# Performance work log

Measured on AMD Instinct MI355X. Metric: run time of the kernel, lower is better.

The kernel has to match this reference:

```python
import jax, jax.numpy as jnp
import numpy as np

N = 50000        # nodes
E = 800000       # edges (avg degree 16)
C_IN = 128
H = 256          # hidden_channels
C_OUT = 128
DEPTH = 4
K = 2            # k_hops -> K+1 = 3 TAGConv weight matrices
L = DEPTH - 1    # residual layers after layer-0 conv
EPS = 1e-5
SLOPE = 0.01     # LeakyReLU default negative slope


def setup_inputs() -> dict:
    key = jax.random.key(0)
    ks = iter(jax.random.split(key, 24))
    s = 0.02
    x = jax.random.normal(next(ks), (N, C_IN), dtype=jnp.float32)
    edge_index = jax.random.randint(next(ks), (2, E), 0, N, dtype=jnp.int64)
    edge_weight = jax.random.uniform(next(ks), (E,), dtype=jnp.float32)
    return {
        'x': x,
        'edge_index': edge_index,
        'edge_weight': edge_weight,
        'W_emb': jax.random.normal(next(ks), (C_IN, H)) * s,
        'b_emb': jnp.zeros((H,), jnp.float32),
        'conv0_W': jax.random.normal(next(ks), (K + 1, H, H)) * s,
        'conv0_b': jnp.zeros((H,), jnp.float32),
        'norm_g': jnp.ones((L, H), jnp.float32),
        'norm_b': jnp.zeros((L, H), jnp.float32),
        'conv_W': jax.random.normal(next(ks), (L, K + 1, H, H)) * s,
        'conv_b': jnp.zeros((L, H), jnp.float32),
        'mlp_W1': jax.random.normal(next(ks), (L, H, 4 * H)) * s,
        'mlp_b1': jnp.zeros((L, 4 * H), jnp.float32),
        'mlp_g': jnp.ones((L, 4 * H), jnp.float32),
        'mlp_bb': jnp.zeros((L, 4 * H), jnp.float32),
        'mlp_W2': jax.random.normal(next(ks), (L, 4 * H, H)) * s,
        'mlp_b2': jnp.zeros((L, H), jnp.float32),
        'W_out': jax.random.normal(next(ks), (H, C_OUT)) * s,
        'b_out': jnp.zeros((C_OUT,), jnp.float32),
    }


def _bn(h, g, b):
    # BatchNorm1d over node dim (training-mode batch statistics)
    m = h.mean(axis=0)
    v = h.var(axis=0)
    return g * (h - m) * jax.lax.rsqrt(v + EPS) + b


def _tagconv(h, src, dst, ew, Ws, b):
    # TAGConv (normalize=False, no self loops): sum_k (A^k h) W_k + b
    out = h @ Ws[0]
    p = h
    for k in range(1, Ws.shape[0]):
        msg = p[src] * ew[:, None]                      # [E, H] gather
        p = jax.ops.segment_sum(msg, dst, num_segments=h.shape[0])
        out = out + p @ Ws[k]
    return out + b


def reference(x, edge_index, edge_weight, W_emb, b_emb, conv0_W, conv0_b,
              norm_g, norm_b, conv_W, conv_b, mlp_W1, mlp_b1, mlp_g, mlp_bb,
              mlp_W2, mlp_b2, W_out, b_out):
    src, dst = edge_index[0], edge_index[1]
    h = x @ W_emb + b_emb                               # x_embed (t=None)
    h = _tagconv(h, src, dst, edge_weight, conv0_W, conv0_b)  # layer-0 conv only
    for l in range(norm_g.shape[0]):                    # res+ blocks
        z = jax.nn.leaky_relu(_bn(h, norm_g[l], norm_b[l]), SLOPE)
        z = _tagconv(z, src, dst, edge_weight, conv_W[l], conv_b[l])
        # pyg MLP [H, 4H, H]: Linear -> BN -> act -> Linear (plain last)
        z = jax.nn.leaky_relu(_bn(z @ mlp_W1[l] + mlp_b1[l], mlp_g[l], mlp_bb[l]), SLOPE)
        z = z @ mlp_W2[l] + mlp_b2[l]
        h = h + z                                       # residual (res=Identity)
    return h @ W_out + b_out
```

## Files before the change

### kernel.cpp

```cpp
#include <hip/hip_runtime.h>

#define HDIM 256
#define EPSV 1e-5f
#define SLOPEV 0.01f

typedef __bf16 bf16;
typedef bf16  bf16x8 __attribute__((ext_vector_type(8)));
typedef bf16  bf16x4 __attribute__((ext_vector_type(4)));
typedef float f32x4  __attribute__((ext_vector_type(4)));

#define GLD16(g, l) __builtin_amdgcn_global_load_lds( \
    (const __attribute__((address_space(1))) void*)(g), \
    (__attribute__((address_space(3))) void*)(l), 16, 0, 0)

template<bool STORE_BF16>
__global__ __launch_bounds__(256)
void gemm_bt_k(const bf16* A0, const bf16* A1, const bf16* A2, const bf16* A3,
               int nseg, int segK,
               const bf16* __restrict__ Wt,
               const float* __restrict__ bias, const bf16* __restrict__ addb,
               void* out0, void* out1, void* out2, void* out3, int ldo,
               int n_store, float* part, int n_stats)
{
    __shared__ char smem[32768];

    const int tid = threadIdx.x;
    const int wave = tid >> 6, lane = tid & 63;
    const int quad = lane >> 4, l16 = lane & 15;
    const int waveM = (wave >> 1) * 64, waveN = (wave & 1) * 64;

    int bid = blockIdx.y * gridDim.x + blockIdx.x;
    const int nwg = gridDim.x * gridDim.y;
    if ((nwg & 7) == 0) {
        const int cpx = nwg >> 3;
        bid = (bid & 7) * cpx + (bid >> 3);
    }
    const int bx = bid % gridDim.x, by = bid / gridDim.x;
    const int bm = by * 128, bn = bx * 128;
    const int K = nseg * segK;

    const bf16* segs[4] = {A0, A1, A2, A3};
    const int srow = tid >> 2;
    const int skof = (tid & 3) * 8;
    char* lAw = smem + wave * 1024;
    char* lBw = smem + 16384 + wave * 1024;

    f32x4 acc[4][4] = {};

    const int spseg = segK >> 5;
    const int T = nseg * spseg;

    auto stage = [&](int s, int kt, int b) {
        const bf16* gA = segs[s] + (size_t)(bm + srow) * segK + kt + skof;
        const bf16* gB = Wt + (size_t)(bn + srow) * K + s * segK + kt + skof;
        char* lA = lAw + b * 8192;
        char* lB = lBw + b * 8192;
        GLD16(gA,                     lA);
        GLD16(gA + (size_t)64 * segK, lA + 4096);
        GLD16(gB,                     lB);
        GLD16(gB + (size_t)64 * K,    lB + 4096);
    };

    stage(0, 0, 0);
    __syncthreads();

    int s = 0, kt = 0;
    for (int t = 0; t < T; ++t) {
        int s2 = s, kt2 = kt + 32;
        if (kt2 == segK) { s2++; kt2 = 0; }
        if (t + 1 < T) stage(s2, kt2, (t + 1) & 1);

        const bf16* pa = (const bf16*)(smem + (t & 1) * 8192)
                         + (waveM + l16) * 32 + quad * 8;
        const bf16* pb = (const bf16*)(smem + 16384 + (t & 1) * 8192)
                         + (waveN + l16) * 32 + quad * 8;
        bf16x8 a0 = *(const bf16x8*)(pa);
        bf16x8 a1 = *(const bf16x8*)(pa + 16 * 32);
        bf16x8 a2 = *(const bf16x8*)(pa + 32 * 32);
        bf16x8 a3 = *(const bf16x8*)(pa + 48 * 32);
        bf16x8 b0 = *(const bf16x8*)(pb);
        bf16x8 b1 = *(const bf16x8*)(pb + 16 * 32);
        bf16x8 b2 = *(const bf16x8*)(pb + 32 * 32);
        bf16x8 b3 = *(const bf16x8*)(pb + 48 * 32);

        acc[0][0] = __builtin_amdgcn_mfma_f32_16x16x32_bf16(a0, b0, acc[0][0], 0, 0, 0);
        acc[0][1] = __builtin_amdgcn_mfma_f32_16x16x32_bf16(a0, b1, acc[0][1], 0, 0, 0);
        acc[0][2] = __builtin_amdgcn_mfma_f32_16x16x32_bf16(a0, b2, acc[0][2], 0, 0, 0);
        acc[0][3] = __builtin_amdgcn_mfma_f32_16x16x32_bf16(a0, b3, acc[0][3], 0, 0, 0);
        acc[1][0] = __builtin_amdgcn_mfma_f32_16x16x32_bf16(a1, b0, acc[1][0], 0, 0, 0);
        acc[1][1] = __builtin_amdgcn_mfma_f32_16x16x32_bf16(a1, b1, acc[1][1], 0, 0, 0);
        acc[1][2] = __builtin_amdgcn_mfma_f32_16x16x32_bf16(a1, b2, acc[1][2], 0, 0, 0);
        acc[1][3] = __builtin_amdgcn_mfma_f32_16x16x32_bf16(a1, b3, acc[1][3], 0, 0, 0);
        acc[2][0] = __builtin_amdgcn_mfma_f32_16x16x32_bf16(a2, b0, acc[2][0], 0, 0, 0);
        acc[2][1] = __builtin_amdgcn_mfma_f32_16x16x32_bf16(a2, b1, acc[2][1], 0, 0, 0);
        acc[2][2] = __builtin_amdgcn_mfma_f32_16x16x32_bf16(a2, b2, acc[2][2], 0, 0, 0);
        acc[2][3] = __builtin_amdgcn_mfma_f32_16x16x32_bf16(a2, b3, acc[2][3], 0, 0, 0);
        acc[3][0] = __builtin_amdgcn_mfma_f32_16x16x32_bf16(a3, b0, acc[3][0], 0, 0, 0);
        acc[3][1] = __builtin_amdgcn_mfma_f32_16x16x32_bf16(a3, b1, acc[3][1], 0, 0, 0);
        acc[3][2] = __builtin_amdgcn_mfma_f32_16x16x32_bf16(a3, b2, acc[3][2], 0, 0, 0);
        acc[3][3] = __builtin_amdgcn_mfma_f32_16x16x32_bf16(a3, b3, acc[3][3], 0, 0, 0);

        __syncthreads();
        s = s2; kt = kt2;
    }

    float bv[4];
#pragma unroll
    for (int j = 0; j < 4; ++j)
        bv[j] = bias ? bias[bn + waveN + j * 16 + l16] : 0.f;
#pragma unroll
    for (int i = 0; i < 4; ++i)
#pragma unroll
        for (int j = 0; j < 4; ++j)
#pragma unroll
            for (int r = 0; r < 4; ++r)
                acc[i][j][r] += bv[j];

    void* outs[4] = {out0, out1, out2, out3};

    if (STORE_BF16) {
        char* stg = smem + wave * 4352;
        float s8[8] = {}, q8[8] = {};
        const int rsel = lane >> 3, csel = lane & 7;
#pragma unroll
        for (int ih = 0; ih < 2; ++ih) {
            __syncthreads();
#pragma unroll
            for (int iw = 0; iw < 2; ++iw) {
                int i = ih * 2 + iw;
#pragma unroll
                for (int j = 0; j < 4; ++j)
#pragma unroll
                    for (int r = 0; r < 4; ++r)
                        *(bf16*)(stg + ((iw * 16 + quad * 4 + r) * 68 + j * 16 + l16) * 2)
                            = (bf16)acc[i][j][r];
            }
            __syncthreads();
#pragma unroll
            for (int rr = 0; rr < 4; ++rr) {
                int rl = rsel + rr * 8;
                bf16x4 lo = *(const bf16x4*)(stg + (rl * 68 + csel * 8) * 2);
                bf16x4 hi = *(const bf16x4*)(stg + (rl * 68 + csel * 8 + 4) * 2);
                int rowg = bm + waveM + ih * 32 + rl;
                int colg = bn + waveN + csel * 8;
                int cseg = colg >> 8, cloc = colg & 255;
                size_t idx = (size_t)rowg * ldo + cloc;
                float f[8];
#pragma unroll
                for (int u = 0; u < 4; ++u) { f[u] = (float)lo[u]; f[4 + u] = (float)hi[u]; }
                if (addb) {
                    bf16x8 o = *(const bf16x8*)(addb + idx);
#pragma unroll
                    for (int u = 0; u < 8; ++u) f[u] += (float)o[u];
                }
                bf16x8 w;
#pragma unroll
                for (int u = 0; u < 8; ++u) w[u] = (bf16)f[u];
                if (rowg < n_store) *(bf16x8*)((bf16*)outs[cseg] + idx) = w;
                if (part && rowg < n_stats) {
#pragma unroll
                    for (int u = 0; u < 8; ++u) { s8[u] += f[u]; q8[u] += f[u] * f[u]; }
                }
            }
        }
        if (part) {
#pragma unroll
            for (int m = 8; m <= 32; m <<= 1)
#pragma unroll
                for (int u = 0; u < 8; ++u) {
                    s8[u] += __shfl_xor(s8[u], m, 64);
                    q8[u] += __shfl_xor(q8[u], m, 64);
                }
            __syncthreads();
            float* Ls = (float*)smem;
            float* Lq = Ls + 256;
            if (rsel == 0) {
#pragma unroll
                for (int u = 0; u < 8; ++u) {
                    Ls[wave * 64 + csel * 8 + u] = s8[u];
                    Lq[wave * 64 + csel * 8 + u] = q8[u];
                }
            }
            __syncthreads();
            if (tid < 128) {
                int hi = tid >> 6, c6 = tid & 63;
                float sv = Ls[hi * 64 + c6] + Ls[(hi + 2) * 64 + c6];
                float qv = Lq[hi * 64 + c6] + Lq[(hi + 2) * 64 + c6];
                int Mtot = gridDim.x * 128;
                int colg = bn + tid;
                part[(size_t)by * Mtot + colg] = sv;
                part[(size_t)(gridDim.y + by) * Mtot + colg] = qv;
            }
        }
    } else {
#pragma unroll
        for (int i = 0; i < 4; ++i)
#pragma unroll
            for (int j = 0; j < 4; ++j) {
                int colg = bn + waveN + j * 16 + l16;
                int cseg = colg >> 8, cloc = colg & 255;
#pragma unroll
                for (int r = 0; r < 4; ++r) {
                    int rowg = bm + waveM + i * 16 + quad * 4 + r;
                    if (rowg < n_store)
                        ((float*)outs[cseg])[(size_t)rowg * ldo + cloc] = acc[i][j][r];
                }
            }
    }
}

__global__ __launch_bounds__(256)
void finalize_k(const float* __restrict__ part, int GY, int M,
                const float* __restrict__ g, const float* __restrict__ bb,
                float* __restrict__ coef, float invn)
{
    const int c = blockIdx.x;
    const int t = threadIdx.x;
    float s = 0.f, q = 0.f;
    const float* ps = part + c;
    const float* pq = part + (size_t)GY * M + c;
    for (int i = t; i < GY; i += 256) {
        s += ps[(size_t)i * M];
        q += pq[(size_t)i * M];
    }
#pragma unroll
    for (int m = 1; m <= 32; m <<= 1) {
        s += __shfl_xor(s, m, 64);
        q += __shfl_xor(q, m, 64);
    }
    __shared__ float Ls[4], Lq[4];
    const int w = t >> 6, l = t & 63;
    if (l == 0) { Ls[w] = s; Lq[w] = q; }
    __syncthreads();
    if (t == 0) {
        s = Ls[0] + Ls[1] + Ls[2] + Ls[3];
        q = Lq[0] + Lq[1] + Lq[2] + Lq[3];
        float mean = s * invn;
        float var  = q * invn - mean * mean;
        float a = g[c] * rsqrtf(var + EPSV);
        coef[c]     = a;
        coef[M + c] = bb[c] - mean * a;
    }
}

__global__ __launch_bounds__(256)
void transpose_cvt_k(const float* __restrict__ src, bf16* __restrict__ dst,
                     int Kseg, int M, int G)
{
    __shared__ float t[32][33];
    const int z = blockIdx.z;
    src += (size_t)z * Kseg * M;
    const int ldd = G * Kseg;
    dst += (size_t)(z / G) * M * ldd + (size_t)(z % G) * Kseg;
    const int tM = blockIdx.x * 32, tK = blockIdx.y * 32;
    const int tx = threadIdx.x & 31, ty = threadIdx.x >> 5;
#pragma unroll
    for (int r = 0; r < 4; ++r)
        t[ty + r * 8][tx] = src[(size_t)(tK + ty + r * 8) * M + tM + tx];
    __syncthreads();
#pragma unroll
    for (int r = 0; r < 4; ++r)
        dst[(size_t)(tM + ty + r * 8) * ldd + tK + tx] = (bf16)t[tx][ty + r * 8];
}

__global__ __launch_bounds__(256)
void cvt_bf_k(const float* __restrict__ src, bf16* __restrict__ dst, long n4)
{
    long i = (long)blockIdx.x * blockDim.x + threadIdx.x;
    if (i >= n4) return;
    float4 v = ((const float4*)src)[i];
    bf16x4 o; o[0] = (bf16)v.x; o[1] = (bf16)v.y; o[2] = (bf16)v.z; o[3] = (bf16)v.w;
    ((bf16x4*)dst)[i] = o;
}

__global__ __launch_bounds__(256)
void deg_k(const int* __restrict__ dst, int* __restrict__ deg, int E)
{
    int e = blockIdx.x * blockDim.x + threadIdx.x;
    if (e < E) atomicAdd(&deg[dst[e]], 1);
}

__global__ __launch_bounds__(256)
void blocksum_k(const int* __restrict__ deg, int* __restrict__ bsum, int N)
{
    int i = blockIdx.x * 256 + threadIdx.x;
    int v = (i < N) ? deg[i] : 0;
#pragma unroll
    for (int m = 1; m <= 32; m <<= 1) v += __shfl_xor(v, m, 64);
    __shared__ int Ls[4];
    if ((threadIdx.x & 63) == 0) Ls[threadIdx.x >> 6] = v;
    __syncthreads();
    if (threadIdx.x == 0) bsum[blockIdx.x] = Ls[0] + Ls[1] + Ls[2] + Ls[3];
}

__global__ __launch_bounds__(256)
void topscan_k(const int* __restrict__ bsum, int* __restrict__ boff, int nb)
{
    __shared__ int s[256];
    int t = threadIdx.x;
    int v = (t < nb) ? bsum[t] : 0;
    s[t] = v;
    __syncthreads();
    for (int off = 1; off < 256; off <<= 1) {
        int u = (t >= off) ? s[t - off] : 0;
        __syncthreads();
        s[t] += u;
        __syncthreads();
    }
    if (t < nb) boff[t] = s[t] - v;
}

__global__ __launch_bounds__(256)
void scatterscan_k(int* __restrict__ deg_wp, const int* __restrict__ boff,
                   int* __restrict__ rowptr, int N)
{
    __shared__ int s[256];
    int t = threadIdx.x;
    int i = blockIdx.x * 256 + t;
    int v = (i < N) ? deg_wp[i] : 0;
    s[t] = v;
    __syncthreads();
    for (int off = 1; off < 256; off <<= 1) {
        int u = (t >= off) ? s[t - off] : 0;
        __syncthreads();
        s[t] += u;
        __syncthreads();
    }
    if (i < N) {
        int incl = s[t] + boff[blockIdx.x];
        rowptr[i + 1] = incl;
        deg_wp[i] = incl - v;
        if (i == 0) rowptr[0] = 0;
    }
}

__global__ __launch_bounds__(256)
void reorder_k(const int* __restrict__ src, const int* __restrict__ dst,
               const float* __restrict__ ew, int* __restrict__ wp,
               int* __restrict__ col, float* __restrict__ wgt, int E)
{
    int e = blockIdx.x * blockDim.x + threadIdx.x;
    if (e >= E) return;
    int d = dst[e];
    int pos = atomicAdd(&wp[d], 1);
    col[pos] = src[e];
    wgt[pos] = ew[e];
}

__global__ __launch_bounds__(256)
void spmm_pull_k(const bf16* __restrict__ P, const int* __restrict__ rowptr,
                 const int* __restrict__ col, const float* __restrict__ wgt,
                 bf16* __restrict__ Q, int N)
{
    int node = blockIdx.x * 8 + (threadIdx.x >> 5);
    int l = threadIdx.x & 31;
    if (node >= N) return;
    int e = rowptr[node], end = rowptr[node + 1];
    float acc[8] = {};
    for (; e + 1 < end; e += 2) {
        int   s0 = col[e], s1 = col[e + 1];
        float w0 = wgt[e], w1 = wgt[e + 1];
        bf16x8 v0 = *(const bf16x8*)(P + (size_t)s0 * HDIM + l * 8);
        bf16x8 v1 = *(const bf16x8*)(P + (size_t)s1 * HDIM + l * 8);
#pragma unroll
        for (int u = 0; u < 8; ++u)
            acc[u] += (float)v0[u] * w0 + (float)v1[u] * w1;
    }
    if (e < end) {
        int s0 = col[e]; float w0 = wgt[e];
        bf16x8 v0 = *(const bf16x8*)(P + (size_t)s0 * HDIM + l * 8);
#pragma unroll
        for (int u = 0; u < 8; ++u) acc[u] += (float)v0[u] * w0;
    }
    bf16x8 o;
#pragma unroll
    for (int u = 0; u < 8; ++u) o[u] = (bf16)acc[u];
    *(bf16x8*)(Q + (size_t)node * HDIM + l * 8) = o;
}

__global__ __launch_bounds__(256)
void apply_bn_k(const bf16* __restrict__ X, const float* __restrict__ coef,
                bf16* __restrict__ Y, int n)
{
    __shared__ float aL[256], bL[256];
    const int tid = threadIdx.x;
    aL[tid] = coef[tid]; bL[tid] = coef[256 + tid];
    __syncthreads();
    long n4 = (long)n * 64;
    for (long i = (long)blockIdx.x * 256 + tid; i < n4; i += (long)gridDim.x * 256) {
        bf16x4 v = ((const bf16x4*)X)[i];
        int c4 = (int)(i & 63) * 4;
        float r0 = fmaf((float)v[0], aL[c4 + 0], bL[c4 + 0]); r0 = r0 > 0.f ? r0 : SLOPEV * r0;
        float r1 = fmaf((float)v[1], aL[c4 + 1], bL[c4 + 1]); r1 = r1 > 0.f ? r1 : SLOPEV * r1;
        float r2 = fmaf((float)v[2], aL[c4 + 2], bL[c4 + 2]); r2 = r2 > 0.f ? r2 : SLOPEV * r2;
        float r3 = fmaf((float)v[3], aL[c4 + 3], bL[c4 + 3]); r3 = r3 > 0.f ? r3 : SLOPEV * r3;
        bf16x4 o; o[0] = (bf16)r0; o[1] = (bf16)r1; o[2] = (bf16)r2; o[3] = (bf16)r3;
        ((bf16x4*)Y)[i] = o;
    }
}

__global__ __launch_bounds__(256)
void apply_bn4_k(bf16* X0, bf16* X1, bf16* X2, bf16* X3,
                 const float* __restrict__ coef, int n)
{
    __shared__ float aL[1024], bL[1024];
    const int tid = threadIdx.x;
#pragma unroll
    for (int q = 0; q < 4; ++q) {
        int c = q * 256 + tid;
        aL[c] = coef[c]; bL[c] = coef[1024 + c];
    }
    __syncthreads();
    bf16* Xs[4] = {X0, X1, X2, X3};
    long per = (long)n * 64;
    long stride = (long)gridDim.x * 256;
    for (int q = 0; q < 4; ++q) {
        bf16* X = Xs[q];
        int cbase = q * 256;
        for (long i = (long)blockIdx.x * 256 + tid; i < per; i += stride) {
            bf16x4 v = ((const bf16x4*)X)[i];
            int c4 = cbase + (int)(i & 63) * 4;
            float r0 = fmaf((float)v[0], aL[c4 + 0], bL[c4 + 0]); r0 = r0 > 0.f ? r0 : SLOPEV * r0;
            float r1 = fmaf((float)v[1], aL[c4 + 1], bL[c4 + 1]); r1 = r1 > 0.f ? r1 : SLOPEV * r1;
            float r2 = fmaf((float)v[2], aL[c4 + 2], bL[c4 + 2]); r2 = r2 > 0.f ? r2 : SLOPEV * r2;
            float r3 = fmaf((float)v[3], aL[c4 + 3], bL[c4 + 3]); r3 = r3 > 0.f ? r3 : SLOPEV * r3;
            bf16x4 o; o[0] = (bf16)r0; o[1] = (bf16)r1; o[2] = (bf16)r2; o[3] = (bf16)r3;
            ((bf16x4*)X)[i] = o;
        }
    }
}

struct GemmArgs {
    const bf16 *A0, *A1, *A2, *A3; int nseg, segK;
    const bf16* Wt; const float* bias; const bf16* addb;
    void *o0, *o1, *o2, *o3; int ldo, M, n_store;
    float* part; int n_stats;
};

static void gemm(hipStream_t st, const GemmArgs& a, int GY, bool store_bf16)
{
    dim3 g(a.M / 128, GY), b(256);
    if (store_bf16)
        gemm_bt_k<true><<<g, b, 0, st>>>(a.A0, a.A1, a.A2, a.A3, a.nseg, a.segK,
            a.Wt, a.bias, a.addb, a.o0, a.o1, a.o2, a.o3, a.ldo, a.n_store,
            a.part, a.n_stats);
    else
        gemm_bt_k<false><<<g, b, 0, st>>>(a.A0, a.A1, a.A2, a.A3, a.nseg, a.segK,
            a.Wt, a.bias, a.addb, a.o0, a.o1, a.o2, a.o3, a.ldo, a.n_store,
            a.part, a.n_stats);
}

extern "C" void kernel_launch(void* const* d_in, const int* in_sizes, int n_in,
                              void* d_out, int out_size, void* d_ws, size_t ws_size,
                              hipStream_t stream)
{
    const float* x       = (const float*)d_in[0];
    const int*   ei      = (const int*)d_in[1];
    const float* ew      = (const float*)d_in[2];
    const float* W_emb   = (const float*)d_in[3];
    const float* b_emb   = (const float*)d_in[4];
    const float* conv0_W = (const float*)d_in[5];
    const float* conv0_b = (const float*)d_in[6];
    const float* norm_g  = (const float*)d_in[7];
    const float* norm_b  = (const float*)d_in[8];
    const float* conv_W  = (const float*)d_in[9];
    const float* conv_b  = (const float*)d_in[10];
    const float* mlp_W1  = (const float*)d_in[11];
    const float* mlp_b1  = (const float*)d_in[12];
    const float* mlp_g   = (const float*)d_in[13];
    const float* mlp_bb  = (const float*)d_in[14];
    const float* mlp_W2  = (const float*)d_in[15];
    const float* mlp_b2  = (const float*)d_in[16];
    const float* W_out   = (const float*)d_in[17];
    const float* b_out   = (const float*)d_in[18];

    const int N = in_sizes[0] / 128;
    const int E = in_sizes[2];
    const int* srcI = ei;
    const int* dstI = ei + E;
    const int N_pad = ((N + 127) / 128) * 128;
    const int GY = N_pad / 128;
    const int NB = (N + 255) / 256;

    const size_t NHp = (size_t)N_pad * HDIM;
    bf16* xb = (bf16*)d_ws;
    bf16* hb = xb + (size_t)N_pad * 128;
    bf16* cb = hb + NHp;
    bf16* p1 = cb + NHp;
    bf16* p2 = p1 + NHp;
    bf16* e1 = p2 + NHp;
    bf16* e2 = e1 + NHp;
    bf16* wa = e2 + NHp;
    bf16* Wt_emb   = wa;
    bf16* Wt_conv0 = wa + 32768;
    bf16* Wt_conv  = wa + 229376;
    bf16* Wt_mlp1  = wa + 819200;
    bf16* Wt_mlp2  = wa + 1605632;
    bf16* Wt_out   = wa + 2392064;
    float* cf_h   = (float*)(wa + 2424832);
    float* cf_m   = cf_h + 512;
    float* partb  = cf_m + 2048;
    int*   rowptr = (int*)(partb + 2 * (size_t)GY * 1024);
    int*   wp     = rowptr + (N + 1);
    int*   col    = wp + N;
    float* wgt    = (float*)(col + E);
    int*   bsum   = (int*)(wgt + E);
    int*   boff   = bsum + 256;

    const float invn = 1.0f / (float)N;
    dim3 pg((N + 7) / 8), pb(256);

    hipMemsetAsync(wp, 0, (size_t)N * 4, stream);
    deg_k<<<dim3((E + 255) / 256), dim3(256), 0, stream>>>(dstI, wp, E);
    blocksum_k<<<dim3(NB), dim3(256), 0, stream>>>(wp, bsum, N);
    topscan_k<<<dim3(1), dim3(256), 0, stream>>>(bsum, boff, NB);
    scatterscan_k<<<dim3(NB), dim3(256), 0, stream>>>(wp, boff, rowptr, N);
    reorder_k<<<dim3((E + 255) / 256), dim3(256), 0, stream>>>(srcI, dstI, ew, wp, col, wgt, E);

    cvt_bf_k<<<dim3((N * 32 + 255) / 256), dim3(256), 0, stream>>>(x, xb, (long)N * 32);
    transpose_cvt_k<<<dim3(8, 4, 1), dim3(256), 0, stream>>>(W_emb, Wt_emb, 128, 256, 1);
    transpose_cvt_k<<<dim3(8, 8, 3), dim3(256), 0, stream>>>(conv0_W, Wt_conv0, 256, 256, 3);
    transpose_cvt_k<<<dim3(8, 8, 9), dim3(256), 0, stream>>>(conv_W, Wt_conv, 256, 256, 3);
    transpose_cvt_k<<<dim3(32, 8, 3), dim3(256), 0, stream>>>(mlp_W1, Wt_mlp1, 256, 1024, 1);
    transpose_cvt_k<<<dim3(8, 32, 3), dim3(256), 0, stream>>>(mlp_W2, Wt_mlp2, 1024, 256, 1);
    transpose_cvt_k<<<dim3(4, 8, 1), dim3(256), 0, stream>>>(W_out, Wt_out, 256, 128, 1);

    {
        GemmArgs a{xb, xb, xb, xb, 1, 128, Wt_emb, b_emb, nullptr,
                   cb, cb, cb, cb, HDIM, 256, N_pad, nullptr, 0};
        gemm(stream, a, GY, true);
    }

    spmm_pull_k<<<pg, pb, 0, stream>>>(cb, rowptr, col, wgt, p1, N);
    spmm_pull_k<<<pg, pb, 0, stream>>>(p1, rowptr, col, wgt, p2, N);
    {
        GemmArgs a{cb, p1, p2, p2, 3, 256, Wt_conv0, conv0_b, nullptr,
                   hb, hb, hb, hb, HDIM, 256, N_pad, partb, N};
        gemm(stream, a, GY, true);
    }
    finalize_k<<<dim3(256), dim3(256), 0, stream>>>(partb, GY, 256, norm_g, norm_b, cf_h, invn);

    for (int l = 0; l < 3; ++l) {
        apply_bn_k<<<dim3(1024), dim3(256), 0, stream>>>(hb, cf_h, e1, N);

        spmm_pull_k<<<pg, pb, 0, stream>>>(e1, rowptr, col, wgt, p1, N);
        spmm_pull_k<<<pg, pb, 0, stream>>>(p1, rowptr, col, wgt, p2, N);
        {
            GemmArgs a{e1, p1, p2, p2, 3, 256, Wt_conv + (size_t)l * 196608,
                       conv_b + l * 256, nullptr, cb, cb, cb, cb, HDIM, 256, N_pad,
                       nullptr, 0};
            gemm(stream, a, GY, true);
        }

        {
            GemmArgs a{cb, cb, cb, cb, 1, 256, Wt_mlp1 + (size_t)l * 262144,
                       mlp_b1 + (size_t)l * 1024, nullptr, p1, p2, e1, e2, HDIM, 1024,
                       N_pad, partb, N};
            gemm(stream, a, GY, true);
        }
        finalize_k<<<dim3(1024), dim3(256), 0, stream>>>(partb, GY, 1024,
                                                         mlp_g + (size_t)l * 1024,
                                                         mlp_bb + (size_t)l * 1024, cf_m, invn);

        apply_bn4_k<<<dim3(2048), dim3(256), 0, stream>>>(p1, p2, e1, e2, cf_m, N);

        {
            GemmArgs a{p1, p2, e1, e2, 4, 256, Wt_mlp2 + (size_t)l * 262144,
                       mlp_b2 + l * 256, hb, hb, hb, hb, hb, HDIM, 256, N_pad,
                       (l < 2) ? partb : nullptr, N};
            gemm(stream, a, GY, true);
        }
        if (l < 2)
            finalize_k<<<dim3(256), dim3(256), 0, stream>>>(partb, GY, 256,
                                                            norm_g + (l + 1) * 256,
                                                            norm_b + (l + 1) * 256, cf_h, invn);
    }

    {
        GemmArgs a{hb, hb, hb, hb, 1, 256, Wt_out, b_out, nullptr,
                   d_out, d_out, d_out, d_out, 128, 128, N, nullptr, 0};
        gemm(stream, a, GY, false);
    }
}
```

Before: 1.394 ms.

## Deepen GEMM LDS pipeline to four stages with explicit vmcnt waits

Replaces the double-buffered LDS staging in the bf16 MFMA GEMM with a 4-buffer ring that keeps three tiles in flight. It uses manual s_waitcnt vmcnt counts and a single barrier per iteration in place of a trailing __syncthreads. It also raises wave priority around the MFMA block. The aim is to hide global-to-LDS load latency better. In exchange LDS per block doubles to 64KB, which may reduce occupancy, and it relies on the ring depth to avoid overwriting a buffer other waves are still reading.

```diff
diff --git a/kernel.cpp b/kernel.cpp
--- a/kernel.cpp
+++ b/kernel.cpp
@@ -22,7 +22,7 @@
                void* out0, void* out1, void* out2, void* out3, int ldo,
                int n_store, float* part, int n_stats)
 {
-    __shared__ char smem[32768];
+    __shared__ char smem[65536];
 
     const int tid = threadIdx.x;
     const int wave = tid >> 6, lane = tid & 63;
@@ -42,37 +42,43 @@
     const bf16* segs[4] = {A0, A1, A2, A3};
     const int srow = tid >> 2;
     const int skof = (tid & 3) * 8;
-    char* lAw = smem + wave * 1024;
-    char* lBw = smem + 16384 + wave * 1024;
 
     f32x4 acc[4][4] = {};
 
-    const int spseg = segK >> 5;
-    const int T = nseg * spseg;
+    const int T = (nseg * segK) >> 5;
 
     auto stage = [&](int s, int kt, int b) {
         const bf16* gA = segs[s] + (size_t)(bm + srow) * segK + kt + skof;
         const bf16* gB = Wt + (size_t)(bn + srow) * K + s * segK + kt + skof;
-        char* lA = lAw + b * 8192;
-        char* lB = lBw + b * 8192;
+        char* lA = smem + b * 8192 + wave * 1024;
+        char* lB = smem + 32768 + b * 8192 + wave * 1024;
         GLD16(gA,                     lA);
         GLD16(gA + (size_t)64 * segK, lA + 4096);
         GLD16(gB,                     lB);
         GLD16(gB + (size_t)64 * K,    lB + 4096);
     };
 
-    stage(0, 0, 0);
-    __syncthreads();
-
-    int s = 0, kt = 0;
+    int ss = 0, kk = 0;
+    for (int i = 0; i < 3; ++i) {
+        stage(ss, kk, i);
+        kk += 32; if (kk == segK) { kk = 0; ++ss; }
+    }
+
     for (int t = 0; t < T; ++t) {
-        int s2 = s, kt2 = kt + 32;
-        if (kt2 == segK) { s2++; kt2 = 0; }
-        if (t + 1 < T) stage(s2, kt2, (t + 1) & 1);
-
-        const bf16* pa = (const bf16*)(smem + (t & 1) * 8192)
+        const int rem = T - t;
+        if (rem >= 3)      asm volatile("s_waitcnt vmcnt(8)" ::: "memory");
+        else if (rem == 2) asm volatile("s_waitcnt vmcnt(4)" ::: "memory");
+        else               asm volatile("s_waitcnt vmcnt(0)" ::: "memory");
+        __builtin_amdgcn_s_barrier();
+
+        if (t + 3 < T) {
+            stage(ss, kk, (t + 3) & 3);
+            kk += 32; if (kk == segK) { kk = 0; ++ss; }
+        }
+
+        const bf16* pa = (const bf16*)(smem + (t & 3) * 8192)
                          + (waveM + l16) * 32 + quad * 8;
-        const bf16* pb = (const bf16*)(smem + 16384 + (t & 1) * 8192)
+        const bf16* pb = (const bf16*)(smem + 32768 + (t & 3) * 8192)
                          + (waveN + l16) * 32 + quad * 8;
         bf16x8 a0 = *(const bf16x8*)(pa);
         bf16x8 a1 = *(const bf16x8*)(pa + 16 * 32);
@@ -83,6 +89,7 @@
         bf16x8 b2 = *(const bf16x8*)(pb + 32 * 32);
         bf16x8 b3 = *(const bf16x8*)(pb + 48 * 32);
 
+        __builtin_amdgcn_s_setprio(1);
         acc[0][0] = __builtin_amdgcn_mfma_f32_16x16x32_bf16(a0, b0, acc[0][0], 0, 0, 0);
         acc[0][1] = __builtin_amdgcn_mfma_f32_16x16x32_bf16(a0, b1, acc[0][1], 0, 0, 0);
         acc[0][2] = __builtin_amdgcn_mfma_f32_16x16x32_bf16(a0, b2, acc[0][2], 0, 0, 0);
@@ -99,9 +106,7 @@
         acc[3][1] = __builtin_amdgcn_mfma_f32_16x16x32_bf16(a3, b1, acc[3][1], 0, 0, 0);
         acc[3][2] = __builtin_amdgcn_mfma_f32_16x16x32_bf16(a3, b2, acc[3][2], 0, 0, 0);
         acc[3][3] = __builtin_amdgcn_mfma_f32_16x16x32_bf16(a3, b3, acc[3][3], 0, 0, 0);
-
-        __syncthreads();
-        s = s2; kt = kt2;
+        __builtin_amdgcn_s_setprio(0);
     }
 
     float bv[4];
```

Result: slower. 1.544 ms (+10.7%).

## Shrink GEMM tile to 128x64, add occupancy hint, and unroll SpMM gather by 4

Applied to the files above, without the earlier changes.

The GEMM kernel's block tile drops from 128x128 to 128x64. This halves the accumulator registers and cuts shared memory to 24KB, and launch_bounds now asks for 4 blocks per CU. The goal is more occupancy and more blocks for latency hiding, at the cost of lower arithmetic intensity and more A-tile reloads. Per-wave epilogue barriers are removed and BN stats become a template parameter. Separately, the SpMM pull loop gets a 4-way unrolled gather so more independent loads are in flight.

```diff
diff --git a/kernel.cpp b/kernel.cpp
--- a/kernel.cpp
+++ b/kernel.cpp
@@ -13,8 +13,8 @@
     (const __attribute__((address_space(1))) void*)(g), \
     (__attribute__((address_space(3))) void*)(l), 16, 0, 0)
 
-template<bool STORE_BF16>
-__global__ __launch_bounds__(256)
+template<bool STORE_BF16, bool STATS>
+__global__ __launch_bounds__(256, 4)
 void gemm_bt_k(const bf16* A0, const bf16* A1, const bf16* A2, const bf16* A3,
                int nseg, int segK,
                const bf16* __restrict__ Wt,
@@ -22,12 +22,12 @@
                void* out0, void* out1, void* out2, void* out3, int ldo,
                int n_store, float* part, int n_stats)
 {
-    __shared__ char smem[32768];
+    __shared__ char smem[24576];
 
     const int tid = threadIdx.x;
     const int wave = tid >> 6, lane = tid & 63;
     const int quad = lane >> 4, l16 = lane & 15;
-    const int waveM = (wave >> 1) * 64, waveN = (wave & 1) * 64;
+    const int waveM = (wave >> 1) * 64, waveN = (wave & 1) * 32;
 
     int bid = blockIdx.y * gridDim.x + blockIdx.x;
     const int nwg = gridDim.x * gridDim.y;
@@ -36,29 +36,25 @@
         bid = (bid & 7) * cpx + (bid >> 3);
     }
     const int bx = bid % gridDim.x, by = bid / gridDim.x;
-    const int bm = by * 128, bn = bx * 128;
+    const int bm = by * 128, bn = bx * 64;
     const int K = nseg * segK;
 
     const bf16* segs[4] = {A0, A1, A2, A3};
     const int srow = tid >> 2;
     const int skof = (tid & 3) * 8;
-    char* lAw = smem + wave * 1024;
-    char* lBw = smem + 16384 + wave * 1024;
-
-    f32x4 acc[4][4] = {};
-
-    const int spseg = segK >> 5;
-    const int T = nseg * spseg;
+
+    f32x4 acc[4][2] = {};
+
+    const int T = K >> 5;
 
     auto stage = [&](int s, int kt, int b) {
         const bf16* gA = segs[s] + (size_t)(bm + srow) * segK + kt + skof;
         const bf16* gB = Wt + (size_t)(bn + srow) * K + s * segK + kt + skof;
-        char* lA = lAw + b * 8192;
-        char* lB = lBw + b * 8192;
+        char* lA = smem + b * 8192 + wave * 1024;
+        char* lB = smem + 16384 + b * 4096 + wave * 1024;
         GLD16(gA,                     lA);
         GLD16(gA + (size_t)64 * segK, lA + 4096);
         GLD16(gB,                     lB);
-        GLD16(gB + (size_t)64 * K,    lB + 4096);
     };
 
     stage(0, 0, 0);
@@ -72,7 +68,7 @@
 
         const bf16* pa = (const bf16*)(smem + (t & 1) * 8192)
                          + (waveM + l16) * 32 + quad * 8;
-        const bf16* pb = (const bf16*)(smem + 16384 + (t & 1) * 8192)
+        const bf16* pb = (const bf16*)(smem + 16384 + (t & 1) * 4096)
                          + (waveN + l16) * 32 + quad * 8;
         bf16x8 a0 = *(const bf16x8*)(pa);
         bf16x8 a1 = *(const bf16x8*)(pa + 16 * 32);
@@ -80,38 +76,28 @@
         bf16x8 a3 = *(const bf16x8*)(pa + 48 * 32);
         bf16x8 b0 = *(const bf16x8*)(pb);
         bf16x8 b1 = *(const bf16x8*)(pb + 16 * 32);
-        bf16x8 b2 = *(const bf16x8*)(pb + 32 * 32);
-        bf16x8 b3 = *(const bf16x8*)(pb + 48 * 32);
 
         acc[0][0] = __builtin_amdgcn_mfma_f32_16x16x32_bf16(a0, b0, acc[0][0], 0, 0, 0);
         acc[0][1] = __builtin_amdgcn_mfma_f32_16x16x32_bf16(a0, b1, acc[0][1], 0, 0, 0);
-        acc[0][2] = __builtin_amdgcn_mfma_f32_16x16x32_bf16(a0, b2, acc[0][2], 0, 0, 0);
-        acc[0][3] = __builtin_amdgcn_mfma_f32_16x16x32_bf16(a0, b3, acc[0][3], 0, 0, 0);
         acc[1][0] = __builtin_amdgcn_mfma_f32_16x16x32_bf16(a1, b0, acc[1][0], 0, 0, 0);
         acc[1][1] = __builtin_amdgcn_mfma_f32_16x16x32_bf16(a1, b1, acc[1][1], 0, 0, 0);
-        acc[1][2] = __builtin_amdgcn_mfma_f32_16x16x32_bf16(a1, b2, acc[1][2], 0, 0, 0);
-        acc[1][3] = __builtin_amdgcn_mfma_f32_16x16x32_bf16(a1, b3, acc[1][3], 0, 0, 0);
         acc[2][0] = __builtin_amdgcn_mfma_f32_16x16x32_bf16(a2, b0, acc[2][0], 0, 0, 0);
         acc[2][1] = __builtin_amdgcn_mfma_f32_16x16x32_bf16(a2, b1, acc[2][1], 0, 0, 0);
-        acc[2][2] = __builtin_amdgcn_mfma_f32_16x16x32_bf16(a2, b2, acc[2][2], 0, 0, 0);
-        acc[2][3] = __builtin_amdgcn_mfma_f32_16x16x32_bf16(a2, b3, acc[2][3], 0, 0, 0);
         acc[3][0] = __builtin_amdgcn_mfma_f32_16x16x32_bf16(a3, b0, acc[3][0], 0, 0, 0);
         acc[3][1] = __builtin_amdgcn_mfma_f32_16x16x32_bf16(a3, b1, acc[3][1], 0, 0, 0);
-        acc[3][2] = __builtin_amdgcn_mfma_f32_16x16x32_bf16(a3, b2, acc[3][2], 0, 0, 0);
-        acc[3][3] = __builtin_amdgcn_mfma_f32_16x16x32_bf16(a3, b3, acc[3][3], 0, 0, 0);
 
         __syncthreads();
         s = s2; kt = kt2;
     }
 
-    float bv[4];
-#pragma unroll
-    for (int j = 0; j < 4; ++j)
+    float bv[2];
+#pragma unroll
+    for (int j = 0; j < 2; ++j)
         bv[j] = bias ? bias[bn + waveN + j * 16 + l16] : 0.f;
 #pragma unroll
     for (int i = 0; i < 4; ++i)
 #pragma unroll
-        for (int j = 0; j < 4; ++j)
+        for (int j = 0; j < 2; ++j)
 #pragma unroll
             for (int r = 0; r < 4; ++r)
                 acc[i][j][r] += bv[j];
@@ -119,35 +105,32 @@
     void* outs[4] = {out0, out1, out2, out3};
 
     if (STORE_BF16) {
-        char* stg = smem + wave * 4352;
+        char* stg = smem + wave * 2560;
         float s8[8] = {}, q8[8] = {};
-        const int rsel = lane >> 3, csel = lane & 7;
+        const int rsel = lane >> 2, csel = lane & 3;
 #pragma unroll
         for (int ih = 0; ih < 2; ++ih) {
-            __syncthreads();
 #pragma unroll
             for (int iw = 0; iw < 2; ++iw) {
                 int i = ih * 2 + iw;
 #pragma unroll
-                for (int j = 0; j < 4; ++j)
+                for (int j = 0; j < 2; ++j)
 #pragma unroll
                     for (int r = 0; r < 4; ++r)
-                        *(bf16*)(stg + ((iw * 16 + quad * 4 + r) * 68 + j * 16 + l16) * 2)
+                        *(bf16*)(stg + ((iw * 16 + quad * 4 + r) * 40 + j * 16 + l16) * 2)
                             = (bf16)acc[i][j][r];
             }
-            __syncthreads();
-#pragma unroll
-            for (int rr = 0; rr < 4; ++rr) {
-                int rl = rsel + rr * 8;
-                bf16x4 lo = *(const bf16x4*)(stg + (rl * 68 + csel * 8) * 2);
-                bf16x4 hi = *(const bf16x4*)(stg + (rl * 68 + csel * 8 + 4) * 2);
+#pragma unroll
+            for (int rr = 0; rr < 2; ++rr) {
+                int rl = rsel + rr * 16;
+                bf16x8 v = *(const bf16x8*)(stg + (rl * 40 + csel * 8) * 2);
                 int rowg = bm + waveM + ih * 32 + rl;
                 int colg = bn + waveN + csel * 8;
                 int cseg = colg >> 8, cloc = colg & 255;
                 size_t idx = (size_t)rowg * ldo + cloc;
                 float f[8];
 #pragma unroll
-                for (int u = 0; u < 4; ++u) { f[u] = (float)lo[u]; f[4 + u] = (float)hi[u]; }
+                for (int u = 0; u < 8; ++u) f[u] = (float)v[u];
                 if (addb) {
                     bf16x8 o = *(const bf16x8*)(addb + idx);
 #pragma unroll
@@ -157,36 +140,35 @@
 #pragma unroll
                 for (int u = 0; u < 8; ++u) w[u] = (bf16)f[u];
                 if (rowg < n_store) *(bf16x8*)((bf16*)outs[cseg] + idx) = w;
-                if (part && rowg < n_stats) {
+                if (STATS && rowg < n_stats) {
 #pragma unroll
                     for (int u = 0; u < 8; ++u) { s8[u] += f[u]; q8[u] += f[u] * f[u]; }
                 }
             }
         }
-        if (part) {
-#pragma unroll
-            for (int m = 8; m <= 32; m <<= 1)
+        if (STATS) {
+#pragma unroll
+            for (int m = 4; m <= 32; m <<= 1)
 #pragma unroll
                 for (int u = 0; u < 8; ++u) {
                     s8[u] += __shfl_xor(s8[u], m, 64);
                     q8[u] += __shfl_xor(q8[u], m, 64);
                 }
-            __syncthreads();
-            float* Ls = (float*)smem;
-            float* Lq = Ls + 256;
+            float* Ls = (float*)(smem + 12288);
+            float* Lq = Ls + 128;
             if (rsel == 0) {
 #pragma unroll
                 for (int u = 0; u < 8; ++u) {
-                    Ls[wave * 64 + csel * 8 + u] = s8[u];
-                    Lq[wave * 64 + csel * 8 + u] = q8[u];
+                    Ls[wave * 32 + csel * 8 + u] = s8[u];
+                    Lq[wave * 32 + csel * 8 + u] = q8[u];
                 }
             }
             __syncthreads();
-            if (tid < 128) {
-                int hi = tid >> 6, c6 = tid & 63;
-                float sv = Ls[hi * 64 + c6] + Ls[(hi + 2) * 64 + c6];
-                float qv = Lq[hi * 64 + c6] + Lq[(hi + 2) * 64 + c6];
-                int Mtot = gridDim.x * 128;
+            if (tid < 64) {
+                int wa = tid >> 5, c5 = tid & 31;
+                float sv = Ls[wa * 32 + c5] + Ls[(wa + 2) * 32 + c5];
+                float qv = Lq[wa * 32 + c5] + Lq[(wa + 2) * 32 + c5];
+                int Mtot = gridDim.x * 64;
                 int colg = bn + tid;
                 part[(size_t)by * Mtot + colg] = sv;
                 part[(size_t)(gridDim.y + by) * Mtot + colg] = qv;
@@ -196,7 +178,7 @@
 #pragma unroll
         for (int i = 0; i < 4; ++i)
 #pragma unroll
-            for (int j = 0; j < 4; ++j) {
+            for (int j = 0; j < 2; ++j) {
                 int colg = bn + waveN + j * 16 + l16;
                 int cseg = colg >> 8, cloc = colg & 255;
 #pragma unroll
@@ -357,6 +339,18 @@
     if (node >= N) return;
     int e = rowptr[node], end = rowptr[node + 1];
     float acc[8] = {};
+    for (; e + 3 < end; e += 4) {
+        int   s0 = col[e],     s1 = col[e + 1], s2 = col[e + 2], s3 = col[e + 3];
+        float w0 = wgt[e],     w1 = wgt[e + 1], w2 = wgt[e + 2], w3 = wgt[e + 3];
+        bf16x8 v0 = *(const bf16x8*)(P + (size_t)s0 * HDIM + l * 8);
+        bf16x8 v1 = *(const bf16x8*)(P + (size_t)s1 * HDIM + l * 8);
+        bf16x8 v2 = *(const bf16x8*)(P + (size_t)s2 * HDIM + l * 8);
+        bf16x8 v3 = *(const bf16x8*)(P + (size_t)s3 * HDIM + l * 8);
+#pragma unroll
+        for (int u = 0; u < 8; ++u)
+            acc[u] += ((float)v0[u] * w0 + (float)v1[u] * w1)
+                    + ((float)v2[u] * w2 + (float)v3[u] * w3);
+    }
     for (; e + 1 < end; e += 2) {
         int   s0 = col[e], s1 = col[e + 1];
         float w0 = wgt[e], w1 = wgt[e + 1];
@@ -437,17 +431,23 @@
     float* part; int n_stats;
 };
 
-static void gemm(hipStream_t st, const GemmArgs& a, int GY, bool store_bf16)
-{
-    dim3 g(a.M / 128, GY), b(256);
-    if (store_bf16)
-        gemm_bt_k<true><<<g, b, 0, st>>>(a.A0, a.A1, a.A2, a.A3, a.nseg, a.segK,
+static void gemm(hipStream_t st, const GemmArgs& a, int GY, bool store_bf16, bool stats)
+{
+    dim3 g(a.M / 64, GY), b(256);
+    if (store_bf16) {
+        if (stats)
+            gemm_bt_k<true, true><<<g, b, 0, st>>>(a.A0, a.A1, a.A2, a.A3, a.nseg, a.segK,
+                a.Wt, a.bias, a.addb, a.o0, a.o1, a.o2, a.o3, a.ldo, a.n_store,
+                a.part, a.n_stats);
+        else
+            gemm_bt_k<true, false><<<g, b, 0, st>>>(a.A0, a.A1, a.A2, a.A3, a.nseg, a.segK,
+                a.Wt, a.bias, a.addb, a.o0, a.o1, a.o2, a.o3, a.ldo, a.n_store,
+                a.part, a.n_stats);
+    } else {
+        gemm_bt_k<false, false><<<g, b, 0, st>>>(a.A0, a.A1, a.A2, a.A3, a.nseg, a.segK,
             a.Wt, a.bias, a.addb, a.o0, a.o1, a.o2, a.o3, a.ldo, a.n_store,
             a.part, a.n_stats);
-    else
-        gemm_bt_k<false><<<g, b, 0, st>>>(a.A0, a.A1, a.A2, a.A3, a.nseg, a.segK,
-            a.Wt, a.bias, a.addb, a.o0, a.o1, a.o2, a.o3, a.ldo, a.n_store,
-            a.part, a.n_stats);
+    }
 }
 
 extern "C" void kernel_launch(void* const* d_in, const int* in_sizes, int n_in,
@@ -528,7 +528,7 @@
     {
         GemmArgs a{xb, xb, xb, xb, 1, 128, Wt_emb, b_emb, nullptr,
                    cb, cb, cb, cb, HDIM, 256, N_pad, nullptr, 0};
-        gemm(stream, a, GY, true);
+        gemm(stream, a, GY, true, false);
     }
 
     spmm_pull_k<<<pg, pb, 0, stream>>>(cb, rowptr, col, wgt, p1, N);
@@ -536,7 +536,7 @@
     {
         GemmArgs a{cb, p1, p2, p2, 3, 256, Wt_conv0, conv0_b, nullptr,
                    hb, hb, hb, hb, HDIM, 256, N_pad, partb, N};
-        gemm(stream, a, GY, true);
+        gemm(stream, a, GY, true, true);
     }
     finalize_k<<<dim3(256), dim3(256), 0, stream>>>(partb, GY, 256, norm_g, norm_b, cf_h, invn);
 
@@ -549,14 +549,14 @@
             GemmArgs a{e1, p1, p2, p2, 3, 256, Wt_conv + (size_t)l * 196608,
                        conv_b + l * 256, nullptr, cb, cb, cb, cb, HDIM, 256, N_pad,
                        nullptr, 0};
-            gemm(stream, a, GY, true);
+            gemm(stream, a, GY, true, false);
         }
 
         {
             GemmArgs a{cb, cb, cb, cb, 1, 256, Wt_mlp1 + (size_t)l * 262144,
                        mlp_b1 + (size_t)l * 1024, nullptr, p1, p2, e1, e2, HDIM, 1024,
                        N_pad, partb, N};
-            gemm(stream, a, GY, true);
+            gemm(stream, a, GY, true, true);
         }
         finalize_k<<<dim3(1024), dim3(256), 0, stream>>>(partb, GY, 1024,
                                                          mlp_g + (size_t)l * 1024,
@@ -568,7 +568,7 @@
             GemmArgs a{p1, p2, e1, e2, 4, 256, Wt_mlp2 + (size_t)l * 262144,
                        mlp_b2 + l * 256, hb, hb, hb, hb, hb, HDIM, 256, N_pad,
                        (l < 2) ? partb : nullptr, N};
-            gemm(stream, a, GY, true);
+            gemm(stream, a, GY, true, l < 2);
         }
         if (l < 2)
             finalize_k<<<dim3(256), dim3(256), 0, stream>>>(partb, GY, 256,
@@ -579,6 +579,6 @@
     {
         GemmArgs a{hb, hb, hb, hb, 1, 256, Wt_out, b_out, nullptr,
                    d_out, d_out, d_out, d_out, 128, 128, N, nullptr, 0};
-        gemm(stream, a, GY, false);
-    }
-}
+        gemm(stream, a, GY, false, false);
+    }
+}
```

Measured after the change: 1.499 ms. +7.5%, slower.
